# Kernel optimization log

Measured on AMD Instinct MI355X. Metric: run time of the kernel, lower is better.

## Reference

```python
import jax, jax.numpy as jnp
import numpy as np

B, N, S = 128, 1024, 2048  # batch, num_neurons, sequence_length


def setup_inputs() -> dict:
    key = jax.random.key(0)
    kx, kw, kb = jax.random.split(key, 3)
    x = jax.random.normal(kx, (B, N, S), dtype=jnp.float32)
    # Stacked per-neuron Linear(seq_len, 1) weights and biases.
    # nn.Linear default init scale: U(-1/sqrt(fan_in), 1/sqrt(fan_in)); we just use scaled normals.
    W = jax.random.normal(kw, (N, S), dtype=jnp.float32) * (1.0 / np.sqrt(S))
    b = jax.random.normal(kb, (N,), dtype=jnp.float32) * (1.0 / np.sqrt(S))
    return {"x": x, "W": W, "b": b}


def reference(x, W, b):
    # Each neuron i computes x[:, i, :] @ W[i] + b[i]; fused into one batched reduction.
    # [B, N, S] x [N, S] -> [B, N]
    return jnp.einsum("bns,ns->bn", x, W) + b
```

## Files before the change

kernel.cpp:

```cpp
#include <hip/hip_runtime.h>
#include <hip/hip_bf16.h>


#define B_DIM 128
#define N_DIM 1024
#define S_DIM 2048

__global__ __launch_bounds__(256) void
neuron_dot_kernel(const float* __restrict__ x,
                  const float* __restrict__ W,
                  const float* __restrict__ bias,
                  float* __restrict__ out) {
    const int wave = threadIdx.x >> 6;
    const int lane = threadIdx.x & 63;
    const long long idx = (long long)blockIdx.x * 4 + wave;
    const int ni = (int)(idx & (N_DIM - 1));

    const float* __restrict__ xr = x + idx * (long long)S_DIM;
    const float* __restrict__ wr = W + (long long)ni * S_DIM;

    float acc = 0.0f;
    #pragma unroll
    for (int it = 0; it < S_DIM / 256; ++it) {
        const int off = it * 256 + lane * 4;
        const float4 xv = *reinterpret_cast<const float4*>(xr + off);
        const float4 wv = *reinterpret_cast<const float4*>(wr + off);
        acc += xv.x * wv.x;
        acc += xv.y * wv.y;
        acc += xv.z * wv.z;
        acc += xv.w * wv.w;
    }

    #pragma unroll
    for (int s = 32; s >= 1; s >>= 1)
        acc += __shfl_xor(acc, s, 64);

    if (lane == 0)
        out[idx] = acc + bias[ni];
}

extern "C" void kernel_launch(void* const* d_in, const int* in_sizes, int n_in,
                              void* d_out, int out_size, void* d_ws, size_t ws_size,
                              hipStream_t stream) {
    const float* x    = (const float*)d_in[0];
    const float* W    = (const float*)d_in[1];
    const float* bias = (const float*)d_in[2];
    float* out        = (float*)d_out;

    const int total_outputs = B_DIM * N_DIM;
    const int blocks = total_outputs / 4;

    neuron_dot_kernel<<<blocks, 256, 0, stream>>>(x, W, bias, out);
}
```

Baseline: 184.5 us.

## Reuse W row in registers across 16 batches with double-buffered nontemporal x loads

```diff
diff --git a/kernel.cpp b/kernel.cpp
--- a/kernel.cpp
+++ b/kernel.cpp
@@ -5,38 +5,71 @@
 #define B_DIM 128
 #define N_DIM 1024
 #define S_DIM 2048
+#define OUTS_PER_WAVE 16
 
-__global__ __launch_bounds__(256) void
+typedef float f32x4 __attribute__((ext_vector_type(4)));
+
+__device__ __forceinline__ f32x4 nt_load4(const float* p) {
+    return __builtin_nontemporal_load(reinterpret_cast<const f32x4*>(p));
+}
+
+__global__ __launch_bounds__(256, 4) void
 neuron_dot_kernel(const float* __restrict__ x,
                   const float* __restrict__ W,
                   const float* __restrict__ bias,
                   float* __restrict__ out) {
     const int wave = threadIdx.x >> 6;
     const int lane = threadIdx.x & 63;
-    const long long idx = (long long)blockIdx.x * 4 + wave;
-    const int ni = (int)(idx & (N_DIM - 1));
+    const int wid  = blockIdx.x * 4 + wave;
+    const int n    = wid & (N_DIM - 1);
+    const int b0   = wid >> 10;
 
-    const float* __restrict__ xr = x + idx * (long long)S_DIM;
-    const float* __restrict__ wr = W + (long long)ni * S_DIM;
+    const float* __restrict__ wr = W + (long long)n * S_DIM;
+    const float bv = bias[n];
 
-    float acc = 0.0f;
+    f32x4 w[8];
     #pragma unroll
-    for (int it = 0; it < S_DIM / 256; ++it) {
-        const int off = it * 256 + lane * 4;
-        const float4 xv = *reinterpret_cast<const float4*>(xr + off);
-        const float4 wv = *reinterpret_cast<const float4*>(wr + off);
-        acc += xv.x * wv.x;
-        acc += xv.y * wv.y;
-        acc += xv.z * wv.z;
-        acc += xv.w * wv.w;
+    for (int it = 0; it < 8; ++it)
+        w[it] = *reinterpret_cast<const f32x4*>(wr + it * 256 + lane * 4);
+
+    const long long xstride = 8LL * N_DIM * S_DIM;
+    const float* xr = x + ((long long)b0 * N_DIM + n) * S_DIM;
+
+    f32x4 buf[2][8];
+    #pragma unroll
+    for (int it = 0; it < 8; ++it)
+        buf[0][it] = nt_load4(xr + it * 256 + lane * 4);
+
+    #pragma unroll 2
+    for (int k = 0; k < OUTS_PER_WAVE; ++k) {
+        const f32x4* cur = buf[k & 1];
+        f32x4*       nxt = buf[(k + 1) & 1];
+
+        if (k + 1 < OUTS_PER_WAVE) {
+            const float* xn = xr + xstride;
+            #pragma unroll
+            for (int it = 0; it < 8; ++it)
+                nxt[it] = nt_load4(xn + it * 256 + lane * 4);
+        }
+
+        float acc = 0.0f;
+        #pragma unroll
+        for (int it = 0; it < 8; ++it) {
+            acc += cur[it][0] * w[it][0];
+            acc += cur[it][1] * w[it][1];
+            acc += cur[it][2] * w[it][2];
+            acc += cur[it][3] * w[it][3];
+        }
+
+        #pragma unroll
+        for (int s = 32; s >= 1; s >>= 1)
+            acc += __shfl_xor(acc, s, 64);
+
+        if (lane == 0)
+            out[(long long)(b0 + 8 * k) * N_DIM + n] = acc + bv;
+
+        xr += xstride;
     }
-
-    #pragma unroll
-    for (int s = 32; s >= 1; s >>= 1)
-        acc += __shfl_xor(acc, s, 64);
-
-    if (lane == 0)
-        out[idx] = acc + bias[ni];
 }
 
 extern "C" void kernel_launch(void* const* d_in, const int* in_sizes, int n_in,
@@ -47,8 +80,6 @@
     const float* bias = (const float*)d_in[2];
     float* out        = (float*)d_out;
 
-    const int total_outputs = B_DIM * N_DIM;
-    const int blocks = total_outputs / 4;
-
+    const int blocks = (B_DIM * N_DIM) / (4 * OUTS_PER_WAVE);
     neuron_dot_kernel<<<blocks, 256, 0, stream>>>(x, W, bias, out);
 }
```

Result: faster. 171.7 us (-6.9%).
